# Kernel tuning notes

Hardware: AMD Instinct MI355X
Metric: run time of the kernel (lower is better)

## Reference

```python
import jax, jax.numpy as jnp
import numpy as np

EPS = 1e-08

def setup_inputs() -> dict:
    key = jax.random.key(0)
    kH, kF, kQ, kK, kV = jax.random.split(key, 5)
    B, N, d = 8192, 16, 512
    H = jax.random.normal(kH, (B, N, d), dtype=jnp.float32)
    F_raw = jax.random.uniform(kF, (B, N), dtype=jnp.float32)
    F = F_raw / jnp.sum(F_raw, axis=-1, keepdims=True)  # fractions sum to 1
    s = 1.0 / np.sqrt(d)
    W_Q = jax.random.normal(kQ, (d, d), dtype=jnp.float32) * s
    W_K = jax.random.normal(kK, (d, d), dtype=jnp.float32) * s
    W_V = jax.random.normal(kV, (d, d), dtype=jnp.float32) * s
    return {"H": H, "F": F, "W_Q": W_Q, "W_K": W_K, "W_V": W_V}

def reference(H, F, W_Q, W_K, W_V):
    d = H.shape[-1]
    scale = jnp.asarray(d, H.dtype) ** 0.5
    # nn.Linear(d, d, bias=False): y = x @ W.T
    Q = jnp.einsum('bnd,ed->bne', H, W_Q)
    K = jnp.einsum('bnd,ed->bne', H, W_K)
    V = jnp.einsum('bnd,ed->bne', H, W_V)
    scores = jnp.einsum('bqd,bkd->bqk', Q, K) / scale  # [B,N,N]
    scores = scores + jnp.log(F + EPS)[:, None, :]      # fraction bias over keys
    alpha = jax.nn.softmax(scores, axis=-1)
    h_attn = jnp.einsum('bqk,bkd->bqd', alpha, V)
    h_out = H + h_attn                                  # residual
    h_poly = jnp.einsum('bn,bnd->bd', F, h_out)         # fraction-weighted pool
    return h_poly
```

## Files before the change

### kernel.cpp

```cpp
#include <hip/hip_runtime.h>

typedef __bf16 bf16x8 __attribute__((ext_vector_type(8)));
typedef float f32x4 __attribute__((ext_vector_type(4)));

__device__ __forceinline__ unsigned short f2bf(float f) {
    unsigned int u = __builtin_bit_cast(unsigned int, f);
    u += 0x7fffu + ((u >> 16) & 1u);
    return (unsigned short)(u >> 16);
}
__device__ __forceinline__ float bf2f(unsigned short u) {
    return __builtin_bit_cast(float, (unsigned)u << 16);
}

__device__ __forceinline__ unsigned swz1k(unsigned byte) {
    return byte ^ ((byte >> 6) & 0x70u);
}

__global__ __launch_bounds__(256) void prep_kernel(
    const float* __restrict__ Wq, const float* __restrict__ Wk,
    const float* __restrict__ Wv, unsigned short* __restrict__ Pc,
    unsigned short* __restrict__ Wvb)
{
    int b = blockIdx.x;
    if (b < 1024) {
        int j0 = (b >> 4) * 8;
        int kc = b & 15;
        int jloc = threadIdx.x >> 5;
        int t = threadIdx.x & 31;
        int j = j0 + jloc, d = kc * 32 + t;
        float acc = 0.f;
        #pragma unroll 8
        for (int e = 0; e < 512; ++e)
            acc = fmaf(Wk[e * 512 + j], Wq[e * 512 + d], acc);
        Pc[((kc * 512) + j) * 32 + t] = f2bf(acc);
    } else {
        int i = (b - 1024) * 256 + (int)threadIdx.x;
        Wvb[i] = f2bf(Wv[i]);
    }
}

__global__ __launch_bounds__(512) void attn_main_kernel(
    const float* __restrict__ H, const float* __restrict__ F,
    const unsigned short* __restrict__ Pc,
    float* __restrict__ out, unsigned short* __restrict__ g_ws)
{
    extern __shared__ char smem[];
    char* HBF = smem;
    char* TBF = smem + 65536;
    float* wbuf = (float*)(smem + 131072);

    const int tid = threadIdx.x;
    const int wv = tid >> 6;
    const int ln = tid & 63;
    const int rl = ln & 15;
    const int kg = ln >> 4;
    const long long gr0 = (long long)blockIdx.x * 64;

    {
        const float4* src = (const float4*)(H + gr0 * 512);
        #pragma unroll
        for (int rep = 0; rep < 16; ++rep) {
            int idx = rep * 512 + tid;
            float4 v = src[idx];
            ushort4 bv;
            bv.x = f2bf(v.x); bv.y = f2bf(v.y); bv.z = f2bf(v.z); bv.w = f2bf(v.w);
            unsigned byte = (unsigned)(idx >> 7) * 1024u + (unsigned)(idx & 127) * 8u;
            *(ushort4*)(HBF + swz1k(byte)) = bv;
        }
    }

    const unsigned short* bptr = Pc + ((wv * 64 + rl) * 32 + kg * 8);

    f32x4 acc[4][4];
    #pragma unroll
    for (int i = 0; i < 4; ++i)
        #pragma unroll
        for (int jj = 0; jj < 4; ++jj)
            acc[i][jj] = f32x4{0.f, 0.f, 0.f, 0.f};

    bf16x8 bcur[4];
    #pragma unroll
    for (int jj = 0; jj < 4; ++jj)
        bcur[jj] = *(const bf16x8*)(bptr + jj * 512);

    __syncthreads();

    #pragma unroll 2
    for (int kc = 0; kc < 16; ++kc) {
        bf16x8 bnext[4];
        if (kc < 15) {
            #pragma unroll
            for (int jj = 0; jj < 4; ++jj)
                bnext[jj] = *(const bf16x8*)(bptr + (kc + 1) * 16384 + jj * 512);
        }
        bf16x8 a[4];
        #pragma unroll
        for (int i = 0; i < 4; ++i) {
            unsigned off = (unsigned)(i * 16 + rl) * 1024u + (unsigned)kc * 64u + (unsigned)kg * 16u;
            a[i] = *(bf16x8*)(HBF + swz1k(off));
        }
        #pragma unroll
        for (int i = 0; i < 4; ++i)
            #pragma unroll
            for (int jj = 0; jj < 4; ++jj)
                acc[i][jj] = __builtin_amdgcn_mfma_f32_16x16x32_bf16(a[i], bcur[jj], acc[i][jj], 0, 0, 0);
        #pragma unroll
        for (int jj = 0; jj < 4; ++jj) bcur[jj] = bnext[jj];
    }

    #pragma unroll
    for (int i = 0; i < 4; ++i)
        #pragma unroll
        for (int jj = 0; jj < 4; ++jj)
            #pragma unroll
            for (int p = 0; p < 4; ++p) {
                unsigned row = (unsigned)(i * 16 + kg * 4 + p);
                unsigned col = (unsigned)(wv * 64 + jj * 16 + rl);
                *(unsigned short*)(TBF + swz1k(row * 1024u + col * 2u)) = f2bf(acc[i][jj][p]);
            }
    __syncthreads();

    if (wv < 4) {
        f32x4 sc = f32x4{0.f, 0.f, 0.f, 0.f};
        #pragma unroll
        for (int kc = 0; kc < 16; ++kc) {
            unsigned off = (unsigned)(wv * 16 + rl) * 1024u + (unsigned)kc * 64u + (unsigned)kg * 16u;
            bf16x8 aT = *(bf16x8*)(TBF + swz1k(off));
            bf16x8 bH = *(bf16x8*)(HBF + swz1k(off));
            sc = __builtin_amdgcn_mfma_f32_16x16x32_bf16(aT, bH, sc, 0, 0, 0);
        }
        const long long Bg = (long long)blockIdx.x * 4 + wv;
        const float* Fb = F + Bg * 16;
        float bias = logf(Fb[rl] + 1e-8f);
        float alpha[4];
        #pragma unroll
        for (int p = 0; p < 4; ++p) {
            float s = sc[p] * 0.044194173824159216f + bias;
            float m = s;
            m = fmaxf(m, __shfl_xor(m, 8));
            m = fmaxf(m, __shfl_xor(m, 4));
            m = fmaxf(m, __shfl_xor(m, 2));
            m = fmaxf(m, __shfl_xor(m, 1));
            float e = expf(s - m);
            float sum = e;
            sum += __shfl_xor(sum, 8);
            sum += __shfl_xor(sum, 4);
            sum += __shfl_xor(sum, 2);
            sum += __shfl_xor(sum, 1);
            alpha[p] = e / sum;
        }
        float part = 0.f;
        #pragma unroll
        for (int p = 0; p < 4; ++p) part += Fb[kg * 4 + p] * alpha[p];
        part += __shfl_xor(part, 16);
        part += __shfl_xor(part, 32);
        if (ln < 16) wbuf[wv * 16 + ln] = part;
    } else {
        int bb = wv - 4;
        const long long Bg = (long long)blockIdx.x * 4 + bb;
        const float* Fb = F + Bg * 16;
        int d0 = ln * 8;
        float o[8];
        #pragma unroll
        for (int q = 0; q < 8; ++q) o[q] = 0.f;
        #pragma unroll
        for (int k = 0; k < 16; ++k) {
            unsigned off = (unsigned)(bb * 16 + k) * 1024u + (unsigned)d0 * 2u;
            ushort4 h0 = *(ushort4*)(HBF + swz1k(off));
            ushort4 h1 = *(ushort4*)(HBF + swz1k(off + 8u));
            float fk = Fb[k];
            o[0] = fmaf(fk, bf2f(h0.x), o[0]); o[1] = fmaf(fk, bf2f(h0.y), o[1]);
            o[2] = fmaf(fk, bf2f(h0.z), o[2]); o[3] = fmaf(fk, bf2f(h0.w), o[3]);
            o[4] = fmaf(fk, bf2f(h1.x), o[4]); o[5] = fmaf(fk, bf2f(h1.y), o[5]);
            o[6] = fmaf(fk, bf2f(h1.z), o[6]); o[7] = fmaf(fk, bf2f(h1.w), o[7]);
        }
        float4 oa; oa.x = o[0]; oa.y = o[1]; oa.z = o[2]; oa.w = o[3];
        float4 ob; ob.x = o[4]; ob.y = o[5]; ob.z = o[6]; ob.w = o[7];
        *(float4*)(out + Bg * 512 + d0) = oa;
        *(float4*)(out + Bg * 512 + d0 + 4) = ob;
    }
    __syncthreads();

    {
        int bb = wv >> 1, dh = wv & 1;
        const long long Bg = (long long)blockIdx.x * 4 + bb;
        int d0 = dh * 256 + ln * 4;
        float g[4];
        #pragma unroll
        for (int q = 0; q < 4; ++q) g[q] = 0.f;
        #pragma unroll
        for (int k = 0; k < 16; ++k) {
            unsigned off = (unsigned)(bb * 16 + k) * 1024u + (unsigned)d0 * 2u;
            ushort4 h = *(ushort4*)(HBF + swz1k(off));
            float wk = wbuf[bb * 16 + k];
            g[0] = fmaf(wk, bf2f(h.x), g[0]); g[1] = fmaf(wk, bf2f(h.y), g[1]);
            g[2] = fmaf(wk, bf2f(h.z), g[2]); g[3] = fmaf(wk, bf2f(h.w), g[3]);
        }
        ushort4 g4; g4.x = f2bf(g[0]); g4.y = f2bf(g[1]); g4.z = f2bf(g[2]); g4.w = f2bf(g[3]);
        *(ushort4*)(g_ws + Bg * 512 + d0) = g4;
    }
}

__global__ __launch_bounds__(256) void out_gemm_kernel(
    const unsigned short* __restrict__ g_ws,
    const unsigned short* __restrict__ Wvb,
    float* __restrict__ out)
{
    extern __shared__ char smem[];
    const int tid = threadIdx.x;
    const int wv = tid >> 6, ln = tid & 63;
    const int rl = ln & 15, kg = ln >> 4;
    const long long r0 = (long long)blockIdx.x * 32;
    {
        const uint4* src = (const uint4*)(g_ws + r0 * 512);
        #pragma unroll
        for (int q = 0; q < 8; ++q) {
            int idx = q * 256 + tid;
            *(uint4*)(smem + swz1k((unsigned)idx * 16u)) = src[idx];
        }
    }
    __syncthreads();
    f32x4 acc[2][8];
    #pragma unroll
    for (int i = 0; i < 2; ++i)
        #pragma unroll
        for (int jj = 0; jj < 8; ++jj)
            acc[i][jj] = f32x4{0.f, 0.f, 0.f, 0.f};
    for (int kc = 0; kc < 16; ++kc) {
        bf16x8 a[2];
        #pragma unroll
        for (int i = 0; i < 2; ++i) {
            unsigned off = (unsigned)(i * 16 + rl) * 1024u + (unsigned)kc * 64u + (unsigned)kg * 16u;
            a[i] = *(bf16x8*)(smem + swz1k(off));
        }
        bf16x8 bfr[8];
        #pragma unroll
        for (int jj = 0; jj < 8; ++jj) {
            int n = wv * 128 + jj * 16 + rl;
            bfr[jj] = *(const bf16x8*)(Wvb + n * 512 + kc * 32 + kg * 8);
        }
        #pragma unroll
        for (int i = 0; i < 2; ++i)
            #pragma unroll
            for (int jj = 0; jj < 8; ++jj)
                acc[i][jj] = __builtin_amdgcn_mfma_f32_16x16x32_bf16(a[i], bfr[jj], acc[i][jj], 0, 0, 0);
    }
    #pragma unroll
    for (int i = 0; i < 2; ++i)
        #pragma unroll
        for (int jj = 0; jj < 8; ++jj)
            #pragma unroll
            for (int p = 0; p < 4; ++p) {
                int row = i * 16 + kg * 4 + p;
                int col = wv * 128 + jj * 16 + rl;
                out[(r0 + row) * 512 + col] += acc[i][jj][p];
            }
}

extern "C" void kernel_launch(void* const* d_in, const int* in_sizes, int n_in,
                              void* d_out, int out_size, void* d_ws, size_t ws_size,
                              hipStream_t stream)
{
    const float* H  = (const float*)d_in[0];
    const float* F  = (const float*)d_in[1];
    const float* Wq = (const float*)d_in[2];
    const float* Wk = (const float*)d_in[3];
    const float* Wv = (const float*)d_in[4];
    float* out = (float*)d_out;

    unsigned short* Pc  = (unsigned short*)d_ws;
    unsigned short* Wvb = Pc + 262144;
    unsigned short* g   = Wvb + 262144;
    (void)in_sizes; (void)n_in; (void)out_size; (void)ws_size;

    hipLaunchKernelGGL(prep_kernel, dim3(2048), dim3(256), 0, stream, Wq, Wk, Wv, Pc, Wvb);
    hipLaunchKernelGGL(attn_main_kernel, dim3(2048), dim3(512), 131328, stream, H, F, Pc, out, g);
    hipLaunchKernelGGL(out_gemm_kernel, dim3(256), dim3(256), 32768, stream, g, Wvb, out);
}
```

Measured before the change: 202.4 us.

## Halve attention block tile to two batches per block for higher occupancy

The main attention kernel now handles 32 rows (2 batch items) per block instead of 64, which halves shared memory to about 64KB and doubles the grid to 4096 blocks. Launch bounds add a min-blocks hint of 4. The point is to fit more blocks per CU so memory latency hides better, at the cost of reloading the Pc projection matrix twice as often per row. The pooling and g-vector phases are remapped across the 8 waves to match the smaller tile.

New measurement: 220.1 us. 8.7% more time.

```diff
diff --git a/kernel.cpp b/kernel.cpp
--- a/kernel.cpp
+++ b/kernel.cpp
@@ -39,27 +39,27 @@
     }
 }
 
-__global__ __launch_bounds__(512) void attn_main_kernel(
+__global__ __launch_bounds__(512, 4) void attn_main_kernel(
     const float* __restrict__ H, const float* __restrict__ F,
     const unsigned short* __restrict__ Pc,
     float* __restrict__ out, unsigned short* __restrict__ g_ws)
 {
     extern __shared__ char smem[];
     char* HBF = smem;
-    char* TBF = smem + 65536;
-    float* wbuf = (float*)(smem + 131072);
+    char* TBF = smem + 32768;
+    float* wbuf = (float*)(smem + 65536);
 
     const int tid = threadIdx.x;
     const int wv = tid >> 6;
     const int ln = tid & 63;
     const int rl = ln & 15;
     const int kg = ln >> 4;
-    const long long gr0 = (long long)blockIdx.x * 64;
+    const long long gr0 = (long long)blockIdx.x * 32;
 
     {
         const float4* src = (const float4*)(H + gr0 * 512);
         #pragma unroll
-        for (int rep = 0; rep < 16; ++rep) {
+        for (int rep = 0; rep < 8; ++rep) {
             int idx = rep * 512 + tid;
             float4 v = src[idx];
             ushort4 bv;
@@ -71,9 +71,9 @@
 
     const unsigned short* bptr = Pc + ((wv * 64 + rl) * 32 + kg * 8);
 
-    f32x4 acc[4][4];
-    #pragma unroll
-    for (int i = 0; i < 4; ++i)
+    f32x4 acc[2][4];
+    #pragma unroll
+    for (int i = 0; i < 2; ++i)
         #pragma unroll
         for (int jj = 0; jj < 4; ++jj)
             acc[i][jj] = f32x4{0.f, 0.f, 0.f, 0.f};
@@ -93,14 +93,14 @@
             for (int jj = 0; jj < 4; ++jj)
                 bnext[jj] = *(const bf16x8*)(bptr + (kc + 1) * 16384 + jj * 512);
         }
-        bf16x8 a[4];
-        #pragma unroll
-        for (int i = 0; i < 4; ++i) {
+        bf16x8 a[2];
+        #pragma unroll
+        for (int i = 0; i < 2; ++i) {
             unsigned off = (unsigned)(i * 16 + rl) * 1024u + (unsigned)kc * 64u + (unsigned)kg * 16u;
             a[i] = *(bf16x8*)(HBF + swz1k(off));
         }
         #pragma unroll
-        for (int i = 0; i < 4; ++i)
+        for (int i = 0; i < 2; ++i)
             #pragma unroll
             for (int jj = 0; jj < 4; ++jj)
                 acc[i][jj] = __builtin_amdgcn_mfma_f32_16x16x32_bf16(a[i], bcur[jj], acc[i][jj], 0, 0, 0);
@@ -109,7 +109,7 @@
     }
 
     #pragma unroll
-    for (int i = 0; i < 4; ++i)
+    for (int i = 0; i < 2; ++i)
         #pragma unroll
         for (int jj = 0; jj < 4; ++jj)
             #pragma unroll
@@ -120,7 +120,7 @@
             }
     __syncthreads();
 
-    if (wv < 4) {
+    if (wv < 2) {
         f32x4 sc = f32x4{0.f, 0.f, 0.f, 0.f};
         #pragma unroll
         for (int kc = 0; kc < 16; ++kc) {
@@ -129,7 +129,7 @@
             bf16x8 bH = *(bf16x8*)(HBF + swz1k(off));
             sc = __builtin_amdgcn_mfma_f32_16x16x32_bf16(aT, bH, sc, 0, 0, 0);
         }
-        const long long Bg = (long long)blockIdx.x * 4 + wv;
+        const long long Bg = (long long)blockIdx.x * 2 + wv;
         const float* Fb = F + Bg * 16;
         float bias = logf(Fb[rl] + 1e-8f);
         float alpha[4];
@@ -155,49 +155,42 @@
         part += __shfl_xor(part, 16);
         part += __shfl_xor(part, 32);
         if (ln < 16) wbuf[wv * 16 + ln] = part;
-    } else {
-        int bb = wv - 4;
-        const long long Bg = (long long)blockIdx.x * 4 + bb;
+    } else if (wv < 6) {
+        int u = wv - 2;
+        int bb = u >> 1, dh = u & 1;
+        const long long Bg = (long long)blockIdx.x * 2 + bb;
         const float* Fb = F + Bg * 16;
-        int d0 = ln * 8;
-        float o[8];
-        #pragma unroll
-        for (int q = 0; q < 8; ++q) o[q] = 0.f;
-        #pragma unroll
-        for (int k = 0; k < 16; ++k) {
-            unsigned off = (unsigned)(bb * 16 + k) * 1024u + (unsigned)d0 * 2u;
-            ushort4 h0 = *(ushort4*)(HBF + swz1k(off));
-            ushort4 h1 = *(ushort4*)(HBF + swz1k(off + 8u));
-            float fk = Fb[k];
-            o[0] = fmaf(fk, bf2f(h0.x), o[0]); o[1] = fmaf(fk, bf2f(h0.y), o[1]);
-            o[2] = fmaf(fk, bf2f(h0.z), o[2]); o[3] = fmaf(fk, bf2f(h0.w), o[3]);
-            o[4] = fmaf(fk, bf2f(h1.x), o[4]); o[5] = fmaf(fk, bf2f(h1.y), o[5]);
-            o[6] = fmaf(fk, bf2f(h1.z), o[6]); o[7] = fmaf(fk, bf2f(h1.w), o[7]);
-        }
-        float4 oa; oa.x = o[0]; oa.y = o[1]; oa.z = o[2]; oa.w = o[3];
-        float4 ob; ob.x = o[4]; ob.y = o[5]; ob.z = o[6]; ob.w = o[7];
-        *(float4*)(out + Bg * 512 + d0) = oa;
-        *(float4*)(out + Bg * 512 + d0 + 4) = ob;
-    }
-    __syncthreads();
-
-    {
-        int bb = wv >> 1, dh = wv & 1;
-        const long long Bg = (long long)blockIdx.x * 4 + bb;
         int d0 = dh * 256 + ln * 4;
-        float g[4];
-        #pragma unroll
-        for (int q = 0; q < 4; ++q) g[q] = 0.f;
+        float o[4];
+        #pragma unroll
+        for (int q = 0; q < 4; ++q) o[q] = 0.f;
         #pragma unroll
         for (int k = 0; k < 16; ++k) {
             unsigned off = (unsigned)(bb * 16 + k) * 1024u + (unsigned)d0 * 2u;
             ushort4 h = *(ushort4*)(HBF + swz1k(off));
+            float fk = Fb[k];
+            o[0] = fmaf(fk, bf2f(h.x), o[0]); o[1] = fmaf(fk, bf2f(h.y), o[1]);
+            o[2] = fmaf(fk, bf2f(h.z), o[2]); o[3] = fmaf(fk, bf2f(h.w), o[3]);
+        }
+        float4 oa; oa.x = o[0]; oa.y = o[1]; oa.z = o[2]; oa.w = o[3];
+        *(float4*)(out + Bg * 512 + d0) = oa;
+    }
+    __syncthreads();
+
+    {
+        int bb = wv >> 2, q4 = wv & 3;
+        const long long Bg = (long long)blockIdx.x * 2 + bb;
+        int d0 = q4 * 128 + ln * 2;
+        float g0 = 0.f, g1 = 0.f;
+        #pragma unroll
+        for (int k = 0; k < 16; ++k) {
+            unsigned off = (unsigned)(bb * 16 + k) * 1024u + (unsigned)d0 * 2u;
+            ushort2 h = *(ushort2*)(HBF + swz1k(off));
             float wk = wbuf[bb * 16 + k];
-            g[0] = fmaf(wk, bf2f(h.x), g[0]); g[1] = fmaf(wk, bf2f(h.y), g[1]);
-            g[2] = fmaf(wk, bf2f(h.z), g[2]); g[3] = fmaf(wk, bf2f(h.w), g[3]);
-        }
-        ushort4 g4; g4.x = f2bf(g[0]); g4.y = f2bf(g[1]); g4.z = f2bf(g[2]); g4.w = f2bf(g[3]);
-        *(ushort4*)(g_ws + Bg * 512 + d0) = g4;
+            g0 = fmaf(wk, bf2f(h.x), g0); g1 = fmaf(wk, bf2f(h.y), g1);
+        }
+        ushort2 g2; g2.x = f2bf(g0); g2.y = f2bf(g1);
+        *(ushort2*)(g_ws + Bg * 512 + d0) = g2;
     }
 }
 
@@ -274,6 +267,6 @@
     (void)in_sizes; (void)n_in; (void)out_size; (void)ws_size;
 
     hipLaunchKernelGGL(prep_kernel, dim3(2048), dim3(256), 0, stream, Wq, Wk, Wv, Pc, Wvb);
-    hipLaunchKernelGGL(attn_main_kernel, dim3(2048), dim3(512), 131328, stream, H, F, Pc, out, g);
+    hipLaunchKernelGGL(attn_main_kernel, dim3(4096), dim3(512), 65664, stream, H, F, Pc, out, g);
     hipLaunchKernelGGL(out_gemm_kernel, dim3(256), dim3(256), 32768, stream, g, Wvb, out);
 }
```

## Split H staging to overlap second-half conversion with first K-half MFMAs, deepen B prefetch

Applied to the files above, without the earlier changes.

The H tile is now loaded entirely into registers up front. Only the first half of the columns is converted to bf16 and stored to LDS before the first eight k-steps run. The second half is written after those MFMAs, so its global-load latency is hidden behind compute. The B-operand prefetch is deepened from one to three stages. F and log(F+eps) are staged once in LDS instead of being re-read from global. Barriers become explicit lgkmcnt waits plus s_barrier, and launch bounds pin one block per CU. The cost is much higher register pressure (16 float4 plus 12 bf16x8 staging registers), which risks spills.

Result: slower. 209.7 us (+3.6%).

```diff
diff --git a/kernel.cpp b/kernel.cpp
--- a/kernel.cpp
+++ b/kernel.cpp
@@ -14,6 +14,10 @@
 
 __device__ __forceinline__ unsigned swz1k(unsigned byte) {
     return byte ^ ((byte >> 6) & 0x70u);
+}
+
+__device__ __forceinline__ void bar_lgkm() {
+    asm volatile("s_waitcnt lgkmcnt(0)\n\ts_barrier" ::: "memory");
 }
 
 __global__ __launch_bounds__(256) void prep_kernel(
@@ -39,7 +43,7 @@
     }
 }
 
-__global__ __launch_bounds__(512) void attn_main_kernel(
+__global__ __launch_bounds__(512, 1) void attn_main_kernel(
     const float* __restrict__ H, const float* __restrict__ F,
     const unsigned short* __restrict__ Pc,
     float* __restrict__ out, unsigned short* __restrict__ g_ws)
@@ -48,6 +52,8 @@
     char* HBF = smem;
     char* TBF = smem + 65536;
     float* wbuf = (float*)(smem + 131072);
+    float* FL   = (float*)(smem + 131328);
+    float* LFL  = (float*)(smem + 131584);
 
     const int tid = threadIdx.x;
     const int wv = tid >> 6;
@@ -56,20 +62,41 @@
     const int kg = ln >> 4;
     const long long gr0 = (long long)blockIdx.x * 64;
 
-    {
-        const float4* src = (const float4*)(H + gr0 * 512);
-        #pragma unroll
-        for (int rep = 0; rep < 16; ++rep) {
-            int idx = rep * 512 + tid;
-            float4 v = src[idx];
-            ushort4 bv;
-            bv.x = f2bf(v.x); bv.y = f2bf(v.y); bv.z = f2bf(v.z); bv.w = f2bf(v.w);
-            unsigned byte = (unsigned)(idx >> 7) * 1024u + (unsigned)(idx & 127) * 8u;
-            *(ushort4*)(HBF + swz1k(byte)) = bv;
-        }
+    float fval = 0.f;
+    if (tid < 64) fval = F[blockIdx.x * 64 + tid];
+
+    const float4* src = (const float4*)(H + gr0 * 512);
+    float4 hreg[16];
+    #pragma unroll
+    for (int rep = 0; rep < 8; ++rep)
+        hreg[rep] = src[(rep * 8 + wv) * 128 + ln];
+    #pragma unroll
+    for (int rep = 0; rep < 8; ++rep)
+        hreg[8 + rep] = src[(rep * 8 + wv) * 128 + 64 + ln];
+
+    if (tid < 64) {
+        FL[tid] = fval;
+        LFL[tid] = logf(fval + 1e-8f);
+    }
+
+    #pragma unroll
+    for (int rep = 0; rep < 8; ++rep) {
+        ushort4 bv;
+        bv.x = f2bf(hreg[rep].x); bv.y = f2bf(hreg[rep].y);
+        bv.z = f2bf(hreg[rep].z); bv.w = f2bf(hreg[rep].w);
+        unsigned byte = (unsigned)(rep * 8 + wv) * 1024u + (unsigned)ln * 8u;
+        *(ushort4*)(HBF + swz1k(byte)) = bv;
     }
 
     const unsigned short* bptr = Pc + ((wv * 64 + rl) * 32 + kg * 8);
+
+    bf16x8 st0[4], st1[4], st2[4];
+    #pragma unroll
+    for (int jj = 0; jj < 4; ++jj) st0[jj] = *(const bf16x8*)(bptr + 0 * 16384 + jj * 512);
+    #pragma unroll
+    for (int jj = 0; jj < 4; ++jj) st1[jj] = *(const bf16x8*)(bptr + 1 * 16384 + jj * 512);
+    #pragma unroll
+    for (int jj = 0; jj < 4; ++jj) st2[jj] = *(const bf16x8*)(bptr + 2 * 16384 + jj * 512);
 
     f32x4 acc[4][4];
     #pragma unroll
@@ -78,21 +105,14 @@
         for (int jj = 0; jj < 4; ++jj)
             acc[i][jj] = f32x4{0.f, 0.f, 0.f, 0.f};
 
-    bf16x8 bcur[4];
-    #pragma unroll
-    for (int jj = 0; jj < 4; ++jj)
-        bcur[jj] = *(const bf16x8*)(bptr + jj * 512);
-
-    __syncthreads();
-
-    #pragma unroll 2
-    for (int kc = 0; kc < 16; ++kc) {
-        bf16x8 bnext[4];
-        if (kc < 15) {
-            #pragma unroll
-            for (int jj = 0; jj < 4; ++jj)
-                bnext[jj] = *(const bf16x8*)(bptr + (kc + 1) * 16384 + jj * 512);
-        }
+    bar_lgkm();
+
+    #pragma unroll
+    for (int kc = 0; kc < 8; ++kc) {
+        bf16x8 bn[4];
+        #pragma unroll
+        for (int jj = 0; jj < 4; ++jj)
+            bn[jj] = *(const bf16x8*)(bptr + (kc + 3) * 16384 + jj * 512);
         bf16x8 a[4];
         #pragma unroll
         for (int i = 0; i < 4; ++i) {
@@ -103,9 +123,42 @@
         for (int i = 0; i < 4; ++i)
             #pragma unroll
             for (int jj = 0; jj < 4; ++jj)
-                acc[i][jj] = __builtin_amdgcn_mfma_f32_16x16x32_bf16(a[i], bcur[jj], acc[i][jj], 0, 0, 0);
-        #pragma unroll
-        for (int jj = 0; jj < 4; ++jj) bcur[jj] = bnext[jj];
+                acc[i][jj] = __builtin_amdgcn_mfma_f32_16x16x32_bf16(a[i], st0[jj], acc[i][jj], 0, 0, 0);
+        #pragma unroll
+        for (int jj = 0; jj < 4; ++jj) { st0[jj] = st1[jj]; st1[jj] = st2[jj]; st2[jj] = bn[jj]; }
+    }
+
+    #pragma unroll
+    for (int rep = 0; rep < 8; ++rep) {
+        ushort4 bv;
+        bv.x = f2bf(hreg[8 + rep].x); bv.y = f2bf(hreg[8 + rep].y);
+        bv.z = f2bf(hreg[8 + rep].z); bv.w = f2bf(hreg[8 + rep].w);
+        unsigned byte = (unsigned)(rep * 8 + wv) * 1024u + (unsigned)(64 + ln) * 8u;
+        *(ushort4*)(HBF + swz1k(byte)) = bv;
+    }
+    bar_lgkm();
+
+    #pragma unroll
+    for (int kc = 8; kc < 16; ++kc) {
+        bf16x8 bn[4];
+        if (kc < 13) {
+            #pragma unroll
+            for (int jj = 0; jj < 4; ++jj)
+                bn[jj] = *(const bf16x8*)(bptr + (kc + 3) * 16384 + jj * 512);
+        }
+        bf16x8 a[4];
+        #pragma unroll
+        for (int i = 0; i < 4; ++i) {
+            unsigned off = (unsigned)(i * 16 + rl) * 1024u + (unsigned)kc * 64u + (unsigned)kg * 16u;
+            a[i] = *(bf16x8*)(HBF + swz1k(off));
+        }
+        #pragma unroll
+        for (int i = 0; i < 4; ++i)
+            #pragma unroll
+            for (int jj = 0; jj < 4; ++jj)
+                acc[i][jj] = __builtin_amdgcn_mfma_f32_16x16x32_bf16(a[i], st0[jj], acc[i][jj], 0, 0, 0);
+        #pragma unroll
+        for (int jj = 0; jj < 4; ++jj) { st0[jj] = st1[jj]; st1[jj] = st2[jj]; st2[jj] = bn[jj]; }
     }
 
     #pragma unroll
@@ -118,7 +171,7 @@
                 unsigned col = (unsigned)(wv * 64 + jj * 16 + rl);
                 *(unsigned short*)(TBF + swz1k(row * 1024u + col * 2u)) = f2bf(acc[i][jj][p]);
             }
-    __syncthreads();
+    bar_lgkm();
 
     if (wv < 4) {
         f32x4 sc = f32x4{0.f, 0.f, 0.f, 0.f};
@@ -129,9 +182,7 @@
             bf16x8 bH = *(bf16x8*)(HBF + swz1k(off));
             sc = __builtin_amdgcn_mfma_f32_16x16x32_bf16(aT, bH, sc, 0, 0, 0);
         }
-        const long long Bg = (long long)blockIdx.x * 4 + wv;
-        const float* Fb = F + Bg * 16;
-        float bias = logf(Fb[rl] + 1e-8f);
+        float bias = LFL[wv * 16 + rl];
         float alpha[4];
         #pragma unroll
         for (int p = 0; p < 4; ++p) {
@@ -151,14 +202,13 @@
         }
         float part = 0.f;
         #pragma unroll
-        for (int p = 0; p < 4; ++p) part += Fb[kg * 4 + p] * alpha[p];
+        for (int p = 0; p < 4; ++p) part += FL[wv * 16 + kg * 4 + p] * alpha[p];
         part += __shfl_xor(part, 16);
         part += __shfl_xor(part, 32);
         if (ln < 16) wbuf[wv * 16 + ln] = part;
     } else {
         int bb = wv - 4;
         const long long Bg = (long long)blockIdx.x * 4 + bb;
-        const float* Fb = F + Bg * 16;
         int d0 = ln * 8;
         float o[8];
         #pragma unroll
@@ -168,7 +218,7 @@
             unsigned off = (unsigned)(bb * 16 + k) * 1024u + (unsigned)d0 * 2u;
             ushort4 h0 = *(ushort4*)(HBF + swz1k(off));
             ushort4 h1 = *(ushort4*)(HBF + swz1k(off + 8u));
-            float fk = Fb[k];
+            float fk = FL[bb * 16 + k];
             o[0] = fmaf(fk, bf2f(h0.x), o[0]); o[1] = fmaf(fk, bf2f(h0.y), o[1]);
             o[2] = fmaf(fk, bf2f(h0.z), o[2]); o[3] = fmaf(fk, bf2f(h0.w), o[3]);
             o[4] = fmaf(fk, bf2f(h1.x), o[4]); o[5] = fmaf(fk, bf2f(h1.y), o[5]);
@@ -179,7 +229,7 @@
         *(float4*)(out + Bg * 512 + d0) = oa;
         *(float4*)(out + Bg * 512 + d0 + 4) = ob;
     }
-    __syncthreads();
+    bar_lgkm();
 
     {
         int bb = wv >> 1, dh = wv & 1;
@@ -274,6 +324,6 @@
     (void)in_sizes; (void)n_in; (void)out_size; (void)ws_size;
 
     hipLaunchKernelGGL(prep_kernel, dim3(2048), dim3(256), 0, stream, Wq, Wk, Wv, Pc, Wvb);
-    hipLaunchKernelGGL(attn_main_kernel, dim3(2048), dim3(512), 131328, stream, H, F, Pc, out, g);
+    hipLaunchKernelGGL(attn_main_kernel, dim3(2048), dim3(512), 131840, stream, H, F, Pc, out, g);
     hipLaunchKernelGGL(out_gemm_kernel, dim3(256), dim3(256), 32768, stream, g, Wvb, out);
 }
```
